# Performance work log

Hardware: AMD Instinct MI355X
Metric: run time of the kernel (lower is better)

The kernel has to match this reference:

```python
import jax, jax.numpy as jnp
import numpy as np

B, C, H, W, D = 16, 512, 14, 14, 8000  # batch, channels(=input_dim1=input_dim2), spatial, output_dim


def _sketch_matrix(seed_h, seed_s, input_dim, output_dim):
    # Reproduce the module's count-sketch matrix generation (np.random.seed based).
    np.random.seed(seed_h)
    rand_h = np.random.randint(output_dim, size=input_dim)
    np.random.seed(seed_s)
    rand_s = (2 * np.random.randint(2, size=input_dim) - 1).astype(np.float32)
    M = np.zeros((input_dim, output_dim), dtype=np.float32)
    M[np.arange(input_dim), rand_h] = rand_s  # one-hot-per-row with sign
    return jnp.asarray(M)


def setup_inputs() -> dict:
    key = jax.random.key(0)
    x = jax.random.normal(key, (B, C, H, W), dtype=jnp.float32)
    S1 = _sketch_matrix(1, 3, C, D)
    S2 = _sketch_matrix(5, 7, C, D)
    return {"x": x, "S1": S1, "S2": S2}


def reference(x, S1, S2):
    b, c, h, w = x.shape
    # NCHW -> (B*H*W, C)
    flat = jnp.transpose(x, (0, 2, 3, 1)).reshape(-1, c)
    sketch1 = flat @ S1  # [BHW, D]
    sketch2 = flat @ S2  # [BHW, D]
    # circular convolution of the two count-sketches via FFT
    f1 = jnp.fft.fft(sketch1, axis=-1)
    f2 = jnp.fft.fft(sketch2, axis=-1)
    cbp_flat = jnp.fft.ifft(f1 * f2, axis=-1).real.astype(x.dtype)
    cbp = cbp_flat.reshape(b, h, w, -1)
    # sum_pool=True: reduce over spatial dims -> [B, D]
    return cbp.sum(axis=(1, 2))
```

## Files before the change

### kernel.cpp

```cpp
#include <hip/hip_runtime.h>

#define B_DIM 16
#define C_DIM 512
#define HW_DIM 196
#define D_DIM 8000
#define KP 224
#define NROW (B_DIM * C_DIM)

typedef __attribute__((ext_vector_type(8))) short short8;
typedef __attribute__((ext_vector_type(4))) float float4v;

__global__ __launch_bounds__(256) void prep(
    const float* __restrict__ x, const float* __restrict__ S1,
    const float* __restrict__ S2,
    int* __restrict__ h, float* __restrict__ s,
    unsigned short* __restrict__ xp) {
    const int bid = blockIdx.x;
    const int tid = threadIdx.x;
    if (bid < 512) {
        __shared__ int found;
        for (int rr = 0; rr < 2; ++rr) {
            const int r     = bid * 2 + rr;
            const int row   = r & (C_DIM - 1);
            const int which = r >> 9;
            const float4* rowp = (const float4*)((which ? S2 : S1) + (size_t)row * D_DIM);
            int*   hp = h + which * C_DIM;
            float* sp = s + which * C_DIM;
            if (tid == 0) found = 0;
            __syncthreads();
            for (int c = 0; c < 8; ++c) {
                int j4 = c * 256 + tid;
                if (j4 < D_DIM / 4) {
                    float4 v = rowp[j4];
                    if (v.x != 0.f) { hp[row] = 4 * j4 + 0; sp[row] = v.x; found = 1; }
                    if (v.y != 0.f) { hp[row] = 4 * j4 + 1; sp[row] = v.y; found = 1; }
                    if (v.z != 0.f) { hp[row] = 4 * j4 + 2; sp[row] = v.z; found = 1; }
                    if (v.w != 0.f) { hp[row] = 4 * j4 + 3; sp[row] = v.w; found = 1; }
                }
                __syncthreads();
                if (found) break;
            }
            __syncthreads();
        }
    } else {
        const int j = bid - 512;
        #pragma unroll
        for (int l = 0; l < 14; ++l) {
            int idx = l * 256 + tid;
            int r   = idx / KP;
            int kk  = idx - r * KP;
            int row = j * 16 + r;
            float v = (kk < HW_DIM) ? x[(size_t)row * HW_DIM + kk] : 0.0f;
            unsigned int u = __float_as_uint(v);
            u = (u + 0x7FFFu + ((u >> 16) & 1u)) >> 16;
            xp[(size_t)row * KP + kk] = (unsigned short)u;
        }
    }
}

__global__ __launch_bounds__(512) void gram_hist(
    const unsigned short* __restrict__ xp,
    const int* __restrict__ h, const float* __restrict__ s,
    float* __restrict__ part) {
    const int jb = blockIdx.x;
    const int ib = blockIdx.y;
    const int b  = blockIdx.z;
    const int tid = threadIdx.x;

    __shared__ __align__(16) float hist[D_DIM];
    #pragma unroll
    for (int l4 = 0; l4 < 4; ++l4) {
        int i4 = l4 * 512 + tid;
        if (i4 < D_DIM / 4)
            ((float4*)hist)[i4] = (float4){0.f, 0.f, 0.f, 0.f};
    }
    __syncthreads();

    const int w  = tid >> 6;
    const int l  = tid & 63;
    const int rA = l & 15;
    const int g  = l >> 4;

    const int i0 = ib * 128 + (w & 3) * 32;
    const int j0 = jb * 128 + (w >> 2) * 64;

    const unsigned short* base = xp + (size_t)b * C_DIM * KP;
    const unsigned short* pA[2];
    const unsigned short* pB[4];
    #pragma unroll
    for (int mt = 0; mt < 2; ++mt)
        pA[mt] = base + (size_t)(i0 + mt * 16 + rA) * KP + g * 8;
    #pragma unroll
    for (int nt = 0; nt < 4; ++nt)
        pB[nt] = base + (size_t)(j0 + nt * 16 + rA) * KP + g * 8;

    float4v acc[2][4];
    #pragma unroll
    for (int mt = 0; mt < 2; ++mt)
        #pragma unroll
        for (int nt = 0; nt < 4; ++nt)
            acc[mt][nt] = (float4v){0.0f, 0.0f, 0.0f, 0.0f};

    short8 fa[2], fb[4];
    #pragma unroll
    for (int mt = 0; mt < 2; ++mt) fa[mt] = *(const short8*)pA[mt];
    #pragma unroll
    for (int nt = 0; nt < 4; ++nt) fb[nt] = *(const short8*)pB[nt];

    #pragma unroll
    for (int step = 1; step <= 7; ++step) {
        short8 na[2], nb[4];
        if (step < 7) {
            #pragma unroll
            for (int mt = 0; mt < 2; ++mt) na[mt] = *(const short8*)(pA[mt] + step * 32);
            #pragma unroll
            for (int nt = 0; nt < 4; ++nt) nb[nt] = *(const short8*)(pB[nt] + step * 32);
        }
        #pragma unroll
        for (int mt = 0; mt < 2; ++mt)
            #pragma unroll
            for (int nt = 0; nt < 4; ++nt)
                acc[mt][nt] = __builtin_amdgcn_mfma_f32_16x16x32_bf16(
                    fa[mt], fb[nt], acc[mt][nt], 0, 0, 0);
        if (step < 7) {
            #pragma unroll
            for (int mt = 0; mt < 2; ++mt) fa[mt] = na[mt];
            #pragma unroll
            for (int nt = 0; nt < 4; ++nt) fb[nt] = nb[nt];
        }
    }

    int hr[2][4]; float sr[2][4]; int hc[4]; float sc[4];
    #pragma unroll
    for (int mt = 0; mt < 2; ++mt)
        #pragma unroll
        for (int rg = 0; rg < 4; ++rg) {
            int c1 = i0 + mt * 16 + (l >> 4) * 4 + rg;
            hr[mt][rg] = h[c1]; sr[mt][rg] = s[c1];
        }
    #pragma unroll
    for (int nt = 0; nt < 4; ++nt) {
        int c2 = j0 + nt * 16 + (l & 15);
        hc[nt] = h[C_DIM + c2]; sc[nt] = s[C_DIM + c2];
    }
    #pragma unroll
    for (int mt = 0; mt < 2; ++mt)
        #pragma unroll
        for (int nt = 0; nt < 4; ++nt)
            #pragma unroll
            for (int rg = 0; rg < 4; ++rg) {
                int bin = hr[mt][rg] + hc[nt];
                if (bin >= D_DIM) bin -= D_DIM;
                atomicAdd(&hist[bin], sr[mt][rg] * sc[nt] * acc[mt][nt][rg]);
            }
    __syncthreads();

    const int slot = b * 16 + ib * 4 + jb;
    float* pb = part + (size_t)slot * D_DIM;
    #pragma unroll
    for (int l4 = 0; l4 < 4; ++l4) {
        int i4 = l4 * 512 + tid;
        if (i4 < D_DIM / 4)
            ((float4*)pb)[i4] = ((const float4*)hist)[i4];
    }
}

__global__ __launch_bounds__(256) void reduce_part(
    const float* __restrict__ part, float* __restrict__ out) {
    int i4 = blockIdx.x * 256 + threadIdx.x;
    if (i4 >= B_DIM * D_DIM / 4) return;
    int b = i4 / (D_DIM / 4);
    int d = i4 - b * (D_DIM / 4);
    const float4* p = (const float4*)(part + (size_t)b * 16 * D_DIM) + d;
    float4 v = {0.f, 0.f, 0.f, 0.f};
    #pragma unroll
    for (int t = 0; t < 16; ++t) {
        float4 q = p[(size_t)t * (D_DIM / 4)];
        v.x += q.x; v.y += q.y; v.z += q.z; v.w += q.w;
    }
    ((float4*)out)[i4] = v;
}

extern "C" void kernel_launch(void* const* d_in, const int* in_sizes, int n_in,
                              void* d_out, int out_size, void* d_ws, size_t ws_size,
                              hipStream_t stream) {
    const float* x  = (const float*)d_in[0];
    const float* S1 = (const float*)d_in[1];
    const float* S2 = (const float*)d_in[2];
    float* out = (float*)d_out;

    int*            h    = (int*)d_ws;
    float*          s    = (float*)(h + 2 * C_DIM);
    unsigned short* xp   = (unsigned short*)(s + 2 * C_DIM);
    float*          part = (float*)(xp + (size_t)NROW * KP);

    prep<<<1024, 256, 0, stream>>>(x, S1, S2, h, s, xp);

    dim3 grid(4, 4, B_DIM);
    gram_hist<<<grid, 512, 0, stream>>>(xp, h, s, part);

    reduce_part<<<(B_DIM * D_DIM / 4 + 255) / 256, 256, 0, stream>>>(part, out);
}
```

Baseline: 116.3 us.

## Replace partial-buffer reduction kernel with global atomics and rebalance prep blocks

Removes the reduce_part kernel and the per-tile partial histogram buffer. Each gram_hist block now atomically adds its nonzero shared-histogram bins straight into the output, which is zeroed inside the prep kernel. Prep is also rebalanced so every block scans one sketch row and converts eight x rows, instead of splitting blocks between the two jobs. This saves one launch and the partial-buffer write and read, at the cost of global atomic contention (16 blocks per batch row) and a non-deterministic summation order.

```diff
diff --git a/kernel.cpp b/kernel.cpp
--- a/kernel.cpp
+++ b/kernel.cpp
@@ -14,54 +14,54 @@
     const float* __restrict__ x, const float* __restrict__ S1,
     const float* __restrict__ S2,
     int* __restrict__ h, float* __restrict__ s,
-    unsigned short* __restrict__ xp) {
+    unsigned short* __restrict__ xp, float* __restrict__ out) {
     const int bid = blockIdx.x;
     const int tid = threadIdx.x;
-    if (bid < 512) {
+
+    {
+        const int row   = bid & (C_DIM - 1);
+        const int which = bid >> 9;
+        const float4* rowp =
+            (const float4*)((which ? S2 : S1) + (size_t)row * D_DIM);
+        int*   hp = h + which * C_DIM;
+        float* sp = s + which * C_DIM;
         __shared__ int found;
-        for (int rr = 0; rr < 2; ++rr) {
-            const int r     = bid * 2 + rr;
-            const int row   = r & (C_DIM - 1);
-            const int which = r >> 9;
-            const float4* rowp = (const float4*)((which ? S2 : S1) + (size_t)row * D_DIM);
-            int*   hp = h + which * C_DIM;
-            float* sp = s + which * C_DIM;
-            if (tid == 0) found = 0;
-            __syncthreads();
-            for (int c = 0; c < 8; ++c) {
-                int j4 = c * 256 + tid;
-                if (j4 < D_DIM / 4) {
-                    float4 v = rowp[j4];
-                    if (v.x != 0.f) { hp[row] = 4 * j4 + 0; sp[row] = v.x; found = 1; }
-                    if (v.y != 0.f) { hp[row] = 4 * j4 + 1; sp[row] = v.y; found = 1; }
-                    if (v.z != 0.f) { hp[row] = 4 * j4 + 2; sp[row] = v.z; found = 1; }
-                    if (v.w != 0.f) { hp[row] = 4 * j4 + 3; sp[row] = v.w; found = 1; }
-                }
-                __syncthreads();
-                if (found) break;
+        if (tid == 0) found = 0;
+        __syncthreads();
+        for (int c = 0; c < 8; ++c) {
+            int j4 = c * 256 + tid;
+            if (j4 < D_DIM / 4) {
+                float4 v = rowp[j4];
+                if (v.x != 0.f) { hp[row] = 4 * j4 + 0; sp[row] = v.x; found = 1; }
+                if (v.y != 0.f) { hp[row] = 4 * j4 + 1; sp[row] = v.y; found = 1; }
+                if (v.z != 0.f) { hp[row] = 4 * j4 + 2; sp[row] = v.z; found = 1; }
+                if (v.w != 0.f) { hp[row] = 4 * j4 + 3; sp[row] = v.w; found = 1; }
             }
             __syncthreads();
-        }
-    } else {
-        const int j = bid - 512;
-        #pragma unroll
-        for (int l = 0; l < 14; ++l) {
-            int idx = l * 256 + tid;
-            int r   = idx / KP;
-            int kk  = idx - r * KP;
-            int row = j * 16 + r;
-            float v = (kk < HW_DIM) ? x[(size_t)row * HW_DIM + kk] : 0.0f;
-            unsigned int u = __float_as_uint(v);
-            u = (u + 0x7FFFu + ((u >> 16) & 1u)) >> 16;
-            xp[(size_t)row * KP + kk] = (unsigned short)u;
+            if (found) break;
         }
     }
+
+    #pragma unroll
+    for (int l = 0; l < 7; ++l) {
+        int idx = l * 256 + tid;
+        int r   = idx / KP;
+        int kk  = idx - r * KP;
+        int row = bid * 8 + r;
+        float v = (kk < HW_DIM) ? x[(size_t)row * HW_DIM + kk] : 0.0f;
+        unsigned int u = __float_as_uint(v);
+        u = (u + 0x7FFFu + ((u >> 16) & 1u)) >> 16;
+        xp[(size_t)row * KP + kk] = (unsigned short)u;
+    }
+
+    if (bid < 1000 && tid < 32)
+        ((float4*)out)[bid * 32 + tid] = (float4){0.f, 0.f, 0.f, 0.f};
 }
 
 __global__ __launch_bounds__(512) void gram_hist(
     const unsigned short* __restrict__ xp,
     const int* __restrict__ h, const float* __restrict__ s,
-    float* __restrict__ part) {
+    float* __restrict__ out) {
     const int jb = blockIdx.x;
     const int ib = blockIdx.y;
     const int b  = blockIdx.z;
@@ -155,30 +155,11 @@
             }
     __syncthreads();
 
-    const int slot = b * 16 + ib * 4 + jb;
-    float* pb = part + (size_t)slot * D_DIM;
-    #pragma unroll
-    for (int l4 = 0; l4 < 4; ++l4) {
-        int i4 = l4 * 512 + tid;
-        if (i4 < D_DIM / 4)
-            ((float4*)pb)[i4] = ((const float4*)hist)[i4];
+    float* ob = out + (size_t)b * D_DIM;
+    for (int i = tid; i < D_DIM; i += 512) {
+        float v = hist[i];
+        if (v != 0.0f) atomicAdd(&ob[i], v);
     }
-}
-
-__global__ __launch_bounds__(256) void reduce_part(
-    const float* __restrict__ part, float* __restrict__ out) {
-    int i4 = blockIdx.x * 256 + threadIdx.x;
-    if (i4 >= B_DIM * D_DIM / 4) return;
-    int b = i4 / (D_DIM / 4);
-    int d = i4 - b * (D_DIM / 4);
-    const float4* p = (const float4*)(part + (size_t)b * 16 * D_DIM) + d;
-    float4 v = {0.f, 0.f, 0.f, 0.f};
-    #pragma unroll
-    for (int t = 0; t < 16; ++t) {
-        float4 q = p[(size_t)t * (D_DIM / 4)];
-        v.x += q.x; v.y += q.y; v.z += q.z; v.w += q.w;
-    }
-    ((float4*)out)[i4] = v;
 }
 
 extern "C" void kernel_launch(void* const* d_in, const int* in_sizes, int n_in,
@@ -189,15 +170,12 @@
     const float* S2 = (const float*)d_in[2];
     float* out = (float*)d_out;
 
-    int*            h    = (int*)d_ws;
-    float*          s    = (float*)(h + 2 * C_DIM);
-    unsigned short* xp   = (unsigned short*)(s + 2 * C_DIM);
-    float*          part = (float*)(xp + (size_t)NROW * KP);
+    int*            h  = (int*)d_ws;
+    float*          s  = (float*)(h + 2 * C_DIM);
+    unsigned short* xp = (unsigned short*)(s + 2 * C_DIM);
 
-    prep<<<1024, 256, 0, stream>>>(x, S1, S2, h, s, xp);
+    prep<<<1024, 256, 0, stream>>>(x, S1, S2, h, s, xp, out);
 
     dim3 grid(4, 4, B_DIM);
-    gram_hist<<<grid, 512, 0, stream>>>(xp, h, s, part);
-
-    reduce_part<<<(B_DIM * D_DIM / 4 + 255) / 256, 256, 0, stream>>>(part, out);
+    gram_hist<<<grid, 512, 0, stream>>>(xp, h, s, out);
 }
```

Result: slower. 118.9 us (+2.3%).
